# Kernel tuning notes

Measured on AMD Instinct MI355X. Metric: run time of the kernel, lower is better.

## Reference

```python
import math
import jax, jax.numpy as jnp
import numpy as np

B, S, D = 2, 2048, 1024
H, DK = 16, 64
NUM_BUCKETS = 32
MAX_DISTANCE = 128


def _relative_position_bucket(relative_position, num_buckets=NUM_BUCKETS, max_distance=MAX_DISTANCE):
    # bidirectional=True branch (encoder / non-causal)
    n = -relative_position
    num_buckets = num_buckets // 2
    ret = (n < 0).astype(jnp.int32) * num_buckets
    n = jnp.abs(n)
    max_exact = num_buckets // 2
    is_small = n < max_exact
    # guard log(0); masked out by is_small anyway
    n_safe = jnp.maximum(n, 1).astype(jnp.float32)
    val_if_large = max_exact + (
        jnp.log(n_safe / max_exact) / math.log(max_distance / max_exact) * (num_buckets - max_exact)
    ).astype(jnp.int32)
    val_if_large = jnp.minimum(val_if_large, num_buckets - 1)
    return ret + jnp.where(is_small, n, val_if_large)


def setup_inputs() -> dict:
    key = jax.random.key(0)
    ks = jax.random.split(key, 6)
    std_q = (D * DK) ** -0.5
    std = D ** -0.5
    return {
        "x": jax.random.normal(ks[0], (B, S, D), jnp.float32),
        "q_w": jax.random.normal(ks[1], (H * DK, D), jnp.float32) * std_q,
        "k_w": jax.random.normal(ks[2], (H * DK, D), jnp.float32) * std,
        "v_w": jax.random.normal(ks[3], (H * DK, D), jnp.float32) * std,
        "o_w": jax.random.normal(ks[4], (D, H * DK), jnp.float32) * ((H * DK) ** -0.5),
        "rel_bias": jax.random.normal(ks[5], (NUM_BUCKETS, H), jnp.float32) * std,
    }


def reference(x, q_w, k_w, v_w, o_w, rel_bias):
    b, s, _ = x.shape
    # project and split heads: [B, H, S, DK]
    def proj(w):
        return (x @ w.T).reshape(b, s, H, DK).transpose(0, 2, 1, 3)
    q, k, v = proj(q_w), proj(k_w), proj(v_w)

    # T5-style unscaled attention scores: [B, H, Sq, Sk]
    scores = jnp.einsum("bhqd,bhkd->bhqk", q, k)

    # bucketed relative-position bias
    ctx = jnp.arange(s)[:, None]
    mem = jnp.arange(s)[None, :]
    rp_bucket = _relative_position_bucket(mem - ctx)  # [S, S]
    bias = rel_bias[rp_bucket]                        # [S, S, H]
    bias = bias.transpose(2, 0, 1)[None]              # [1, H, S, S]
    scores = scores + bias

    attn = jax.nn.softmax(scores, axis=-1)
    ctx_out = jnp.einsum("bhqk,bhkd->bhqd", attn, v)
    ctx_out = ctx_out.transpose(0, 2, 1, 3).reshape(b, s, H * DK)
    return ctx_out @ o_w.T
```

## Files before the change

kernel.cpp:

```cpp
#include <hip/hip_runtime.h>
#include <stdint.h>


typedef unsigned short u16;
typedef __attribute__((ext_vector_type(8))) short short8;
typedef __attribute__((ext_vector_type(4))) float float4v;
typedef __attribute__((ext_vector_type(4))) u16 ushort4v;
typedef __attribute__((ext_vector_type(4))) uint32_t uint4v;

typedef __attribute__((address_space(1))) void void_g;
typedef __attribute__((address_space(3))) void void_l;

#define L2E 1.4426950408889634f

__device__ __forceinline__ u16 f2b(float f) {
  union { float f; uint32_t u; } v; v.f = f;
  uint32_t r = (v.u + 0x7fffu + ((v.u >> 16) & 1u)) >> 16;
  return (u16)r;
}
__device__ __forceinline__ u16 f2b_fast(float f) {
  union { float f; uint32_t u; } v; v.f = f;
  return (u16)((v.u + 0x8000u) >> 16);
}

__global__ void cvt_all(const float* __restrict__ x,  const float* __restrict__ qw,
                        const float* __restrict__ kw, const float* __restrict__ vw,
                        const float* __restrict__ ow, const float* __restrict__ rel_bias,
                        u16* __restrict__ xb, u16* __restrict__ wqkv, u16* __restrict__ owb,
                        float* __restrict__ biasT) {
  int bi = blockIdx.x;
  if (bi >= 8192) {
    int idx = (bi - 8192) * 256 + threadIdx.x;
    int h = idx >> 12, t = idx & 4095;
    if (t > 4094) { biasT[h * 4096 + 4095] = -1.0e4f; return; }
    int d = t - 2047;
    int n = -d;
    int ret = (n < 0) ? 16 : 0;
    int na = (n < 0) ? -n : n;
    int bucket;
    if (na < 8) {
      bucket = ret + na;
    } else {
      float v = logf((float)na / 8.0f) / logf(16.0f) * 8.0f;
      int vi = 8 + (int)v;
      bucket = ret + (vi > 15 ? 15 : vi);
    }
    biasT[h * 4096 + t] = (rel_bias[bucket * 16 + h] - 8.0f) * L2E;
    return;
  }
  int i = bi * 256 + threadIdx.x;
  const float* s; u16* d; int off;
  if (i < 1048576)      { s = x;  d = xb;              off = i; }
  else if (i < 1310720) { s = qw; d = wqkv;            off = i - 1048576; }
  else if (i < 1572864) { s = kw; d = wqkv + 1048576;  off = i - 1310720; }
  else if (i < 1835008) { s = vw; d = wqkv + 2097152;  off = i - 1572864; }
  else                  { s = ow; d = owb;             off = i - 1835008; }
  float4v v = ((const float4v*)s)[off];
  ushort4v o;
  o.x = f2b(v.x); o.y = f2b(v.y); o.z = f2b(v.z); o.w = f2b(v.w);
  ((ushort4v*)d)[off] = o;
}

__global__ __launch_bounds__(256, 2)
void gemm_qkv(const u16* __restrict__ A, const u16* __restrict__ W,
              u16* __restrict__ qkb, u16* __restrict__ vTp) {
  const int K = 1024;
  __shared__ __align__(16) char SM[34816];
  u16* As = (u16*)SM;
  u16* Bs = (u16*)(SM + 16384);
  const int tid = threadIdx.x;
  const int wid = tid >> 6;
  const int lane = tid & 63;
  const int row16 = lane & 15, oct = lane >> 4;
  const int tm = blockIdx.x * 128, tn = blockIdx.y * 128;
  const int wm = (wid & 1) * 64, wn = (wid >> 1) * 64;
  const int srow = lane >> 2;
  const int sc = (lane & 3) * 8;
  float4v acc[4][4] = {};
  for (int k0 = 0; k0 < K; k0 += 64) {
    __syncthreads();
#pragma unroll
    for (int i = 0; i < 4; i++) {
      const int idx = i * 4 + wid;
      const int kk = idx & 1;
      const int rb = idx >> 1;
      const int r = rb * 16 + srow;
      const int c = kk * 32 + sc;
      __builtin_amdgcn_global_load_lds((void_g*)(A + (size_t)(tm + r) * K + k0 + c),
                                       (void_l*)(As + (kk * 128 + rb * 16) * 32), 16, 0, 0);
      __builtin_amdgcn_global_load_lds((void_g*)(W + (size_t)(tn + r) * K + k0 + c),
                                       (void_l*)(Bs + (kk * 128 + rb * 16) * 32), 16, 0, 0);
    }
    __syncthreads();
#pragma unroll
    for (int kk = 0; kk < 2; kk++) {
      short8 af[4], bfr[4];
#pragma unroll
      for (int mi = 0; mi < 4; mi++)
        af[mi] = *(const short8*)(As + (kk * 128 + wm + mi * 16 + row16) * 32 + oct * 8);
#pragma unroll
      for (int ni = 0; ni < 4; ni++)
        bfr[ni] = *(const short8*)(Bs + (kk * 128 + wn + ni * 16 + row16) * 32 + oct * 8);
#pragma unroll
      for (int mi = 0; mi < 4; mi++)
#pragma unroll
        for (int ni = 0; ni < 4; ni++)
          acc[mi][ni] = __builtin_amdgcn_mfma_f32_16x16x32_bf16(af[mi], bfr[ni], acc[mi][ni], 0, 0, 0);
    }
  }

  u16* Es = (u16*)SM;
  __syncthreads();
#pragma unroll
  for (int mi = 0; mi < 4; mi++)
#pragma unroll
    for (int ni = 0; ni < 4; ni++)
#pragma unroll
      for (int r = 0; r < 4; r++)
        Es[(wm + mi * 16 + oct * 4 + r) * 136 + wn + ni * 16 + row16] = f2b(acc[mi][ni][r]);
  __syncthreads();

  if (tn < 2048) {
#pragma unroll
    for (int it = 0; it < 8; it++) {
      int idx = it * 256 + tid;
      int row = idx >> 4, c = idx & 15;
      short8 v = *(const short8*)(Es + row * 136 + c * 8);
      *(short8*)(qkb + (size_t)(tm + row) * 2048 + tn + c * 8) = v;
    }
  } else {
    const int h0 = (tn - 2048) >> 6;
    const int b = tm >> 11;
    const int s0 = tm & 2047;
#pragma unroll
    for (int it = 0; it < 8; it++) {
      int idx = it * 256 + tid;
      int dg = idx >> 4;
      int ch = idx & 15;
      short8 o;
#pragma unroll
      for (int j = 0; j < 8; j++) {
        int sp = ch * 8 + j;
        int sl = (sp & ~31) + (((sp >> 2) & 1) << 4) + (((sp >> 3) & 3) << 2) + (sp & 3);
        o[j] = (short)Es[sl * 136 + dg];
      }
      const int head = h0 + (dg >> 6), d = dg & 63;
      *(short8*)(vTp + ((size_t)((b * 16 + head) * 64 + d)) * 2048 + s0 + ch * 8) = o;
    }
  }
}

__global__ __launch_bounds__(256, 2)
void gemm_out(const u16* __restrict__ A, const u16* __restrict__ W,
              float* __restrict__ C) {
  const int K = 1024, N = 1024;
  __shared__ __align__(16) char SM[34816];
  u16* As = (u16*)SM;
  u16* Bs = (u16*)(SM + 16384);
  const int tid = threadIdx.x;
  const int wid = tid >> 6;
  const int lane = tid & 63;
  const int row16 = lane & 15, oct = lane >> 4;
  const int tm = blockIdx.x * 128, tn = blockIdx.y * 128;
  const int wm = (wid & 1) * 64, wn = (wid >> 1) * 64;
  const int srow = lane >> 2;
  const int sc = (lane & 3) * 8;
  float4v acc[4][4] = {};
  for (int k0 = 0; k0 < K; k0 += 64) {
    __syncthreads();
#pragma unroll
    for (int i = 0; i < 4; i++) {
      const int idx = i * 4 + wid;
      const int kk = idx & 1;
      const int rb = idx >> 1;
      const int r = rb * 16 + srow;
      const int c = kk * 32 + sc;
      __builtin_amdgcn_global_load_lds((void_g*)(A + (size_t)(tm + r) * K + k0 + c),
                                       (void_l*)(As + (kk * 128 + rb * 16) * 32), 16, 0, 0);
      __builtin_amdgcn_global_load_lds((void_g*)(W + (size_t)(tn + r) * K + k0 + c),
                                       (void_l*)(Bs + (kk * 128 + rb * 16) * 32), 16, 0, 0);
    }
    __syncthreads();
#pragma unroll
    for (int kk = 0; kk < 2; kk++) {
      short8 af[4], bfr[4];
#pragma unroll
      for (int mi = 0; mi < 4; mi++)
        af[mi] = *(const short8*)(As + (kk * 128 + wm + mi * 16 + row16) * 32 + oct * 8);
#pragma unroll
      for (int ni = 0; ni < 4; ni++)
        bfr[ni] = *(const short8*)(Bs + (kk * 128 + wn + ni * 16 + row16) * 32 + oct * 8);
#pragma unroll
      for (int mi = 0; mi < 4; mi++)
#pragma unroll
        for (int ni = 0; ni < 4; ni++)
          acc[mi][ni] = __builtin_amdgcn_mfma_f32_16x16x32_bf16(af[mi], bfr[ni], acc[mi][ni], 0, 0, 0);
    }
  }
  float* Ef = (float*)SM;
#pragma unroll
  for (int pass = 0; pass < 2; pass++) {
    __syncthreads();
    if ((wid & 1) == pass) {
#pragma unroll
      for (int mi = 0; mi < 4; mi++)
#pragma unroll
        for (int ni = 0; ni < 4; ni++)
#pragma unroll
          for (int r = 0; r < 4; r++)
            Ef[(mi * 16 + oct * 4 + r) * 132 + wn + ni * 16 + row16] = acc[mi][ni][r];
    }
    __syncthreads();
#pragma unroll
    for (int it = 0; it < 8; it++) {
      int idx = it * 256 + tid;
      int row = idx >> 5, c = idx & 31;
      float4v v = *(const float4v*)(Ef + row * 132 + c * 4);
      *(float4v*)(C + (size_t)(tm + pass * 64 + row) * N + tn + c * 4) = v;
    }
  }
}

__global__ __launch_bounds__(256, 2)
void flash_attn(const u16* __restrict__ qkb, const u16* __restrict__ vTp,
                const float* __restrict__ biasT, u16* __restrict__ ctx) {
  const int S = 2048, LDQ = 2048;
  const int qt0 = blockIdx.x * 128;
  const int h = blockIdx.y, b = blockIdx.z;
  const int tid = threadIdx.x, wid = tid >> 6, lane = tid & 63;
  const int row16 = lane & 15, oct = lane >> 4;

  __shared__ __align__(16) float biasS[2176];
  __shared__ __align__(16) u16 Ks[2][64][40];
  __shared__ __align__(16) u16 Vts[2][64][40];

  {
    const float* bsrc = biasT + h * 4096 + (1920 - qt0);
    for (int i = tid; i < 544; i += 256)
      ((float4v*)biasS)[i] = ((const float4v*)bsrc)[i];
  }
  const float bias_neg = biasT[h * 4096];
  const float bias_pos = biasT[h * 4096 + 4094];

  const u16* qbase = qkb + ((size_t)b * S + qt0 + wid * 32) * LDQ + h * 64;
  short8 qf[2][2];
#pragma unroll
  for (int f = 0; f < 2; f++)
#pragma unroll
    for (int hd = 0; hd < 2; hd++)
      qf[f][hd] = *(const short8*)(qbase + (size_t)(f * 16 + row16) * LDQ + hd * 32 + oct * 8);

  float lsum[2] = {};
  float4v o_acc[2][4] = {};

  const int sr = lane >> 2, c8 = (lane & 3) * 8;
  const int srow = wid * 16 + sr;
  const u16* Kst = qkb + 1024 + ((size_t)b * S + srow) * LDQ + c8 + h * 64;
  const u16* Vst = vTp + ((size_t)(b * 16 + h) * 64 + srow) * 2048 + c8;

  short8 kreg[2], vreg[2];
#pragma unroll
  for (int hd = 0; hd < 2; hd++) kreg[hd] = *(const short8*)(Kst + hd * 32);
#pragma unroll
  for (int ks = 0; ks < 2; ks++) vreg[ks] = *(const short8*)(Vst + ks * 32);

  for (int kt = 0; kt < S; kt += 64) {
    __syncthreads();
#pragma unroll
    for (int hd = 0; hd < 2; hd++) *(short8*)&Ks[hd][srow][c8] = kreg[hd];
#pragma unroll
    for (int ks = 0; ks < 2; ks++) *(short8*)&Vts[ks][srow][c8] = vreg[ks];
    __syncthreads();

    if (kt + 64 < S) {
#pragma unroll
      for (int hd = 0; hd < 2; hd++)
        kreg[hd] = *(const short8*)(Kst + (size_t)(kt + 64) * LDQ + hd * 32);
#pragma unroll
      for (int ks = 0; ks < 2; ks++)
        vreg[ks] = *(const short8*)(Vst + (kt + 64) + ks * 32);
    }

    short8 kf[4][2];
#pragma unroll
    for (int st = 0; st < 4; st++)
#pragma unroll
      for (int hd = 0; hd < 2; hd++)
        kf[st][hd] = *(const short8*)&Ks[hd][st * 16 + row16][oct * 8];

    float4v sc[2][4];
#pragma unroll
    for (int f = 0; f < 2; f++)
#pragma unroll
      for (int st = 0; st < 4; st++) {
        float4v s = {};
        s = __builtin_amdgcn_mfma_f32_16x16x32_bf16(kf[st][0], qf[f][0], s, 0, 0, 0);
        s = __builtin_amdgcn_mfma_f32_16x16x32_bf16(kf[st][1], qf[f][1], s, 0, 0, 0);
        sc[f][st] = s;
      }

    short8 vf[2][4];
#pragma unroll
    for (int ks = 0; ks < 2; ks++)
#pragma unroll
      for (int ni = 0; ni < 4; ni++)
        vf[ks][ni] = *(const short8*)&Vts[ks][ni * 16 + row16][oct * 8];

    const int dk = kt - qt0;
    const bool far = (dk >= 256) || (dk <= -192);
    if (far) {
      const float bc = (dk > 0) ? bias_pos : bias_neg;
#pragma unroll
      for (int f = 0; f < 2; f++)
#pragma unroll
        for (int st = 0; st < 4; st++)
#pragma unroll
          for (int r = 0; r < 4; r++)
            sc[f][st][r] = __builtin_amdgcn_exp2f(__builtin_fmaf(sc[f][st][r], L2E, bc));
    } else {
#pragma unroll
      for (int f = 0; f < 2; f++) {
        const int basef = kt + oct * 4 - wid * 32 - f * 16 - row16 + 127;
#pragma unroll
        for (int st = 0; st < 4; st++)
#pragma unroll
          for (int r = 0; r < 4; r++)
            sc[f][st][r] = __builtin_amdgcn_exp2f(
                __builtin_fmaf(sc[f][st][r], L2E, biasS[basef + st * 16 + r]));
      }
    }

#pragma unroll
    for (int f = 0; f < 2; f++) {
      lsum[f] += ((sc[f][0][0] + sc[f][0][1]) + (sc[f][0][2] + sc[f][0][3])) +
                 ((sc[f][1][0] + sc[f][1][1]) + (sc[f][1][2] + sc[f][1][3])) +
                 ((sc[f][2][0] + sc[f][2][1]) + (sc[f][2][2] + sc[f][2][3])) +
                 ((sc[f][3][0] + sc[f][3][1]) + (sc[f][3][2] + sc[f][3][3]));
#pragma unroll
      for (int ks = 0; ks < 2; ks++) {
        uint4v pw;
        pw.x = (uint32_t)f2b_fast(sc[f][2 * ks][0]) | ((uint32_t)f2b_fast(sc[f][2 * ks][1]) << 16);
        pw.y = (uint32_t)f2b_fast(sc[f][2 * ks][2]) | ((uint32_t)f2b_fast(sc[f][2 * ks][3]) << 16);
        pw.z = (uint32_t)f2b_fast(sc[f][2 * ks + 1][0]) | ((uint32_t)f2b_fast(sc[f][2 * ks + 1][1]) << 16);
        pw.w = (uint32_t)f2b_fast(sc[f][2 * ks + 1][2]) | ((uint32_t)f2b_fast(sc[f][2 * ks + 1][3]) << 16);
        short8 pf = __builtin_bit_cast(short8, pw);
#pragma unroll
        for (int ni = 0; ni < 4; ni++)
          o_acc[f][ni] = __builtin_amdgcn_mfma_f32_16x16x32_bf16(pf, vf[ks][ni], o_acc[f][ni], 0, 0, 0);
      }
    }
  }

#pragma unroll
  for (int f = 0; f < 2; f++) {
    float v = lsum[f];
    v += __shfl_xor(v, 16);
    v += __shfl_xor(v, 32);
    float linv[4];
#pragma unroll
    for (int r = 0; r < 4; r++)
      linv[r] = 1.0f / __shfl(v, ((lane >> 4) << 2) + r);
    const size_t orow = (size_t)b * S + qt0 + wid * 32 + f * 16 + oct * 4;
#pragma unroll
    for (int ni = 0; ni < 4; ni++)
#pragma unroll
      for (int r = 0; r < 4; r++)
        ctx[(orow + r) * 1024 + h * 64 + ni * 16 + row16] = f2b_fast(o_acc[f][ni][r] * linv[r]);
  }
}

extern "C" void kernel_launch(void* const* d_in, const int* in_sizes, int n_in,
                              void* d_out, int out_size, void* d_ws, size_t ws_size,
                              hipStream_t stream) {
  const float* x        = (const float*)d_in[0];
  const float* q_w      = (const float*)d_in[1];
  const float* k_w      = (const float*)d_in[2];
  const float* v_w      = (const float*)d_in[3];
  const float* o_w      = (const float*)d_in[4];
  const float* rel_bias = (const float*)d_in[5];

  char* ws = (char*)d_ws;
  u16*   xb    = (u16*)(ws);
  u16*   wqkv  = (u16*)(ws + 8388608);
  u16*   owb   = (u16*)(ws + 14680064);
  u16*   qkb   = (u16*)(ws + 16777216);
  u16*   vTp   = (u16*)(ws + 33554432);
  u16*   ctxb  = (u16*)(ws + 41943040);
  float* biasT = (float*)(ws + 50331648);

  cvt_all<<<8448, 256, 0, stream>>>(x, q_w, k_w, v_w, o_w, rel_bias,
                                    xb, wqkv, owb, biasT);

  dim3 g1(4096 / 128, 3072 / 128);
  gemm_qkv<<<g1, 256, 0, stream>>>(xb, wqkv, qkb, vTp);

  dim3 g2(2048 / 128, 16, 2);
  flash_attn<<<g2, 256, 0, stream>>>(qkb, vTp, biasT, ctxb);

  dim3 g3(4096 / 128, 1024 / 128);
  gemm_out<<<g3, 256, 0, stream>>>(ctxb, owb, (float*)d_out);
}
```

Baseline: 191.4 us.

## Shrink out-GEMM tiles, remap attention blocks, MFMA row sums, setprio

The output GEMM moves from 128x128 to 64x128 tiles, which doubles the block count for better CU occupancy and simplifies the epilogue to a single pass. The attention kernel remaps the linear block index to interleave heads and query tiles across XCDs for L2 locality. It also computes the softmax row sums with an extra MFMA against a ones vector instead of scalar adds and shuffles, and raises wave priority around the MFMA sections. The trade-offs are more redundant W loads in the GEMM and one extra MFMA per P tile in attention.

```diff
diff --git a/kernel.cpp b/kernel.cpp
--- a/kernel.cpp
+++ b/kernel.cpp
@@ -156,18 +156,28 @@
   const int K = 1024, N = 1024;
   __shared__ __align__(16) char SM[34816];
   u16* As = (u16*)SM;
-  u16* Bs = (u16*)(SM + 16384);
+  u16* Bs = (u16*)(SM + 8192);
   const int tid = threadIdx.x;
   const int wid = tid >> 6;
   const int lane = tid & 63;
   const int row16 = lane & 15, oct = lane >> 4;
-  const int tm = blockIdx.x * 128, tn = blockIdx.y * 128;
-  const int wm = (wid & 1) * 64, wn = (wid >> 1) * 64;
+  const int tm = blockIdx.x * 64, tn = blockIdx.y * 128;
+  const int wm = (wid & 1) * 32, wn = (wid >> 1) * 64;
   const int srow = lane >> 2;
   const int sc = (lane & 3) * 8;
-  float4v acc[4][4] = {};
+  float4v acc[2][4] = {};
   for (int k0 = 0; k0 < K; k0 += 64) {
     __syncthreads();
+#pragma unroll
+    for (int i = 0; i < 2; i++) {
+      const int idx = i * 4 + wid;
+      const int kk = idx & 1;
+      const int rb = idx >> 1;
+      const int r = rb * 16 + srow;
+      const int c = kk * 32 + sc;
+      __builtin_amdgcn_global_load_lds((void_g*)(A + (size_t)(tm + r) * K + k0 + c),
+                                       (void_l*)(As + (kk * 64 + rb * 16) * 32), 16, 0, 0);
+    }
 #pragma unroll
     for (int i = 0; i < 4; i++) {
       const int idx = i * 4 + wid;
@@ -175,49 +185,42 @@
       const int rb = idx >> 1;
       const int r = rb * 16 + srow;
       const int c = kk * 32 + sc;
-      __builtin_amdgcn_global_load_lds((void_g*)(A + (size_t)(tm + r) * K + k0 + c),
-                                       (void_l*)(As + (kk * 128 + rb * 16) * 32), 16, 0, 0);
       __builtin_amdgcn_global_load_lds((void_g*)(W + (size_t)(tn + r) * K + k0 + c),
                                        (void_l*)(Bs + (kk * 128 + rb * 16) * 32), 16, 0, 0);
     }
     __syncthreads();
 #pragma unroll
     for (int kk = 0; kk < 2; kk++) {
-      short8 af[4], bfr[4];
-#pragma unroll
-      for (int mi = 0; mi < 4; mi++)
-        af[mi] = *(const short8*)(As + (kk * 128 + wm + mi * 16 + row16) * 32 + oct * 8);
+      short8 af[2], bfr[4];
+#pragma unroll
+      for (int mi = 0; mi < 2; mi++)
+        af[mi] = *(const short8*)(As + (kk * 64 + wm + mi * 16 + row16) * 32 + oct * 8);
 #pragma unroll
       for (int ni = 0; ni < 4; ni++)
         bfr[ni] = *(const short8*)(Bs + (kk * 128 + wn + ni * 16 + row16) * 32 + oct * 8);
 #pragma unroll
-      for (int mi = 0; mi < 4; mi++)
+      for (int mi = 0; mi < 2; mi++)
 #pragma unroll
         for (int ni = 0; ni < 4; ni++)
           acc[mi][ni] = __builtin_amdgcn_mfma_f32_16x16x32_bf16(af[mi], bfr[ni], acc[mi][ni], 0, 0, 0);
     }
   }
   float* Ef = (float*)SM;
-#pragma unroll
-  for (int pass = 0; pass < 2; pass++) {
-    __syncthreads();
-    if ((wid & 1) == pass) {
-#pragma unroll
-      for (int mi = 0; mi < 4; mi++)
-#pragma unroll
-        for (int ni = 0; ni < 4; ni++)
-#pragma unroll
-          for (int r = 0; r < 4; r++)
-            Ef[(mi * 16 + oct * 4 + r) * 132 + wn + ni * 16 + row16] = acc[mi][ni][r];
-    }
-    __syncthreads();
-#pragma unroll
-    for (int it = 0; it < 8; it++) {
-      int idx = it * 256 + tid;
-      int row = idx >> 5, c = idx & 31;
-      float4v v = *(const float4v*)(Ef + row * 132 + c * 4);
-      *(float4v*)(C + (size_t)(tm + pass * 64 + row) * N + tn + c * 4) = v;
-    }
+  __syncthreads();
+#pragma unroll
+  for (int mi = 0; mi < 2; mi++)
+#pragma unroll
+    for (int ni = 0; ni < 4; ni++)
+#pragma unroll
+      for (int r = 0; r < 4; r++)
+        Ef[(wm + mi * 16 + oct * 4 + r) * 132 + wn + ni * 16 + row16] = acc[mi][ni][r];
+  __syncthreads();
+#pragma unroll
+  for (int it = 0; it < 8; it++) {
+    int idx = it * 256 + tid;
+    int row = idx >> 5, c = idx & 31;
+    float4v v = *(const float4v*)(Ef + row * 132 + c * 4);
+    *(float4v*)(C + (size_t)(tm + row) * N + tn + c * 4) = v;
   }
 }
 
@@ -225,8 +228,10 @@
 void flash_attn(const u16* __restrict__ qkb, const u16* __restrict__ vTp,
                 const float* __restrict__ biasT, u16* __restrict__ ctx) {
   const int S = 2048, LDQ = 2048;
-  const int qt0 = blockIdx.x * 128;
-  const int h = blockIdx.y, b = blockIdx.z;
+  const int lin = blockIdx.x + (blockIdx.y << 4) + (blockIdx.z << 8);
+  const int V = (lin & 7) * 64 + (lin >> 3);
+  const int qt0 = (V & 15) * 128;
+  const int h = (V >> 4) & 15, b = V >> 8;
   const int tid = threadIdx.x, wid = tid >> 6, lane = tid & 63;
   const int row16 = lane & 15, oct = lane >> 4;
 
@@ -250,8 +255,9 @@
     for (int hd = 0; hd < 2; hd++)
       qf[f][hd] = *(const short8*)(qbase + (size_t)(f * 16 + row16) * LDQ + hd * 32 + oct * 8);
 
-  float lsum[2] = {};
+  float4v l_acc[2] = {};
   float4v o_acc[2][4] = {};
+  const short8 ones = {0x3F80, 0x3F80, 0x3F80, 0x3F80, 0x3F80, 0x3F80, 0x3F80, 0x3F80};
 
   const int sr = lane >> 2, c8 = (lane & 3) * 8;
   const int srow = wid * 16 + sr;
@@ -289,6 +295,7 @@
         kf[st][hd] = *(const short8*)&Ks[hd][st * 16 + row16][oct * 8];
 
     float4v sc[2][4];
+    __builtin_amdgcn_s_setprio(1);
 #pragma unroll
     for (int f = 0; f < 2; f++)
 #pragma unroll
@@ -298,6 +305,7 @@
         s = __builtin_amdgcn_mfma_f32_16x16x32_bf16(kf[st][1], qf[f][1], s, 0, 0, 0);
         sc[f][st] = s;
       }
+    __builtin_amdgcn_s_setprio(0);
 
     short8 vf[2][4];
 #pragma unroll
@@ -332,10 +340,6 @@
 
 #pragma unroll
     for (int f = 0; f < 2; f++) {
-      lsum[f] += ((sc[f][0][0] + sc[f][0][1]) + (sc[f][0][2] + sc[f][0][3])) +
-                 ((sc[f][1][0] + sc[f][1][1]) + (sc[f][1][2] + sc[f][1][3])) +
-                 ((sc[f][2][0] + sc[f][2][1]) + (sc[f][2][2] + sc[f][2][3])) +
-                 ((sc[f][3][0] + sc[f][3][1]) + (sc[f][3][2] + sc[f][3][3]));
 #pragma unroll
       for (int ks = 0; ks < 2; ks++) {
         uint4v pw;
@@ -344,22 +348,22 @@
         pw.z = (uint32_t)f2b_fast(sc[f][2 * ks + 1][0]) | ((uint32_t)f2b_fast(sc[f][2 * ks + 1][1]) << 16);
         pw.w = (uint32_t)f2b_fast(sc[f][2 * ks + 1][2]) | ((uint32_t)f2b_fast(sc[f][2 * ks + 1][3]) << 16);
         short8 pf = __builtin_bit_cast(short8, pw);
+        __builtin_amdgcn_s_setprio(1);
 #pragma unroll
         for (int ni = 0; ni < 4; ni++)
           o_acc[f][ni] = __builtin_amdgcn_mfma_f32_16x16x32_bf16(pf, vf[ks][ni], o_acc[f][ni], 0, 0, 0);
+        l_acc[f] = __builtin_amdgcn_mfma_f32_16x16x32_bf16(pf, ones, l_acc[f], 0, 0, 0);
+        __builtin_amdgcn_s_setprio(0);
       }
     }
   }
 
 #pragma unroll
   for (int f = 0; f < 2; f++) {
-    float v = lsum[f];
-    v += __shfl_xor(v, 16);
-    v += __shfl_xor(v, 32);
     float linv[4];
 #pragma unroll
     for (int r = 0; r < 4; r++)
-      linv[r] = 1.0f / __shfl(v, ((lane >> 4) << 2) + r);
+      linv[r] = 1.0f / l_acc[f][r];
     const size_t orow = (size_t)b * S + qt0 + wid * 32 + f * 16 + oct * 4;
 #pragma unroll
     for (int ni = 0; ni < 4; ni++)
@@ -397,6 +401,6 @@
   dim3 g2(2048 / 128, 16, 2);
   flash_attn<<<g2, 256, 0, stream>>>(qkb, vTp, biasT, ctxb);
 
-  dim3 g3(4096 / 128, 1024 / 128);
+  dim3 g3(4096 / 64, 1024 / 128);
   gemm_out<<<g3, 256, 0, stream>>>(ctxb, owb, (float*)d_out);
 }
```

Result: faster. 181.3 us (-5.3%).
